# Optimization experiments

Hardware: AMD Instinct MI355X
Metric: run time of the kernel (lower is better)

## Reference

```python
import jax, jax.numpy as jnp
import numpy as np

H = 32        # query heads
KV = 8        # key/value heads
D = 128       # head_dim
GROUPS = H // KV
THETA = 10000.0


def _rope_cos_sin(position_ids):
    # position_ids: [B, S] int
    inv_freq = 1.0 / (THETA ** (jnp.arange(0, D, 2, dtype=jnp.float32) / D))  # [D/2]
    freqs = position_ids.astype(jnp.float32)[:, :, None] * inv_freq[None, None, :]  # [B,S,D/2]
    emb = jnp.concatenate([freqs, freqs], axis=-1)  # [B,S,D]
    return jnp.cos(emb), jnp.sin(emb)


def _rotate_half(x):
    x1, x2 = jnp.split(x, 2, axis=-1)
    return jnp.concatenate([-x2, x1], axis=-1)


def _apply_rope(x, cos, sin):
    # x: [B,h,S,D]; cos/sin: [B,S,D] -> broadcast over heads
    return x * cos[:, None, :, :] + _rotate_half(x) * sin[:, None, :, :]


def setup_inputs() -> dict:
    key = jax.random.key(0)
    ks = jax.random.split(key, 8)
    B, S, Dm = 2, 2048, 4096
    scale = lambda d: 1.0 / np.sqrt(d)
    hidden_states = jax.random.normal(ks[0], (B, S, Dm), dtype=jnp.float32)
    position_ids = jnp.broadcast_to(jnp.arange(S, dtype=jnp.int32)[None, :], (B, S))
    Wq = jax.random.normal(ks[1], (Dm, H * D), dtype=jnp.float32) * scale(Dm)
    Wk = jax.random.normal(ks[2], (Dm, KV * D), dtype=jnp.float32) * scale(Dm)
    Wv = jax.random.normal(ks[3], (Dm, KV * D), dtype=jnp.float32) * scale(Dm)
    Wo = jax.random.normal(ks[4], (H * D, Dm), dtype=jnp.float32) * scale(H * D)
    # per-head shift-encoder correction weights (small init so it's a correction)
    Ws_q = jax.random.normal(ks[5], (H, D, D), dtype=jnp.float32) * (0.02 * scale(D))
    Ws_k = jax.random.normal(ks[6], (H, D, D), dtype=jnp.float32) * (0.02 * scale(D))
    return {"hidden_states": hidden_states, "position_ids": position_ids,
            "Wq": Wq, "Wk": Wk, "Wv": Wv, "Wo": Wo, "Ws_q": Ws_q, "Ws_k": Ws_k}


def reference(hidden_states, position_ids, Wq, Wk, Wv, Wo, Ws_q, Ws_k):
    B, S, Dm = hidden_states.shape
    # projections -> [B, heads, S, D]
    q = (hidden_states @ Wq).reshape(B, S, H, D).transpose(0, 2, 1, 3)
    k = (hidden_states @ Wk).reshape(B, S, KV, D).transpose(0, 2, 1, 3)
    v = (hidden_states @ Wv).reshape(B, S, KV, D).transpose(0, 2, 1, 3)
    # RoPE
    cos, sin = _rope_cos_sin(position_ids)
    q = _apply_rope(q, cos, sin)
    k = _apply_rope(k, cos, sin)
    # GQA repeat_kv: [B,KV,S,D] -> [B,H,S,D]
    k = jnp.repeat(k, GROUPS, axis=1)
    v = jnp.repeat(v, GROUPS, axis=1)
    # causal SDPA
    scores = jnp.einsum('bhqd,bhkd->bhqk', q, k) / jnp.sqrt(jnp.float32(D))
    causal = jnp.tril(jnp.ones((S, S), dtype=bool))
    scores = jnp.where(causal[None, None, :, :], scores, jnp.float32(-1e30))
    probs = jax.nn.softmax(scores, axis=-1)
    attn = jnp.einsum('bhqk,bhkd->bhqd', probs, v)  # [B,H,S,D]
    attn = attn.transpose(0, 2, 1, 3)               # [B,S,H,D]
    # shift_encoder.do_shift: per-head linear correction from rotated Q and K
    delta = jnp.einsum('bhsd,hde->bshe', q, Ws_q) + jnp.einsum('bhsd,hde->bshe', k, Ws_k)
    attn = attn + delta
    # output projection
    out = attn.reshape(B, S, H * D) @ Wo
    return out
```

## Files before the change

### kernel.cpp

```cpp
#include <hip/hip_runtime.h>
#include <cstdint>

#define DEV __device__ __forceinline__

typedef __attribute__((ext_vector_type(4))) float  f32x4;
typedef __attribute__((ext_vector_type(8))) short  s16x8;
typedef __attribute__((ext_vector_type(4))) unsigned short u16x4;
typedef __attribute__((ext_vector_type(8))) unsigned short u16x8;

constexpr int B_   = 2;
constexpr int S_   = 2048;
constexpr int DM   = 4096;
constexpr int HQ   = 32;
constexpr int KVH  = 8;
constexpr int DH   = 128;
constexpr int NQKV = 6144;

DEV unsigned short f2bf(float f) {
  union { float f; unsigned u; } c; c.f = f;
  unsigned u = c.u + 0x7FFFu + ((c.u >> 16) & 1u);
  return (unsigned short)(u >> 16);
}
DEV float bf2f(unsigned short h) {
  union { unsigned u; float f; } c; c.u = (unsigned)h << 16; return c.f;
}
DEV void gload16(const void* g, const void* l) {
  __builtin_amdgcn_global_load_lds(
      (const __attribute__((address_space(1))) unsigned int*)(uintptr_t)g,
      (__attribute__((address_space(3))) unsigned int*)(unsigned)(uintptr_t)l,
      16, 0, 0);
}
DEV f32x4 mfma16x16(s16x8 a, s16x8 b, f32x4 c) {
  return __builtin_amdgcn_mfma_f32_16x16x32_bf16(a, b, c, 0, 0, 0);
}

__global__ __launch_bounds__(256) void k_tables(const int* __restrict__ pos,
                                                float* __restrict__ ct,
                                                float* __restrict__ st) {
  int i = blockIdx.x * 256 + threadIdx.x;
  if (i >= B_ * S_ * 64) return;
  int f = i & 63, bs = i >> 6;
  float p   = (float)pos[bs];
  float inv = __builtin_amdgcn_exp2f(-(float)f * 0.20762050593048355f);
  float a   = p * inv;
  ct[i] = cosf(a);
  st[i] = sinf(a);
}

__global__ __launch_bounds__(256) void k_cvt(const float* __restrict__ in,
                                             unsigned short* __restrict__ out,
                                             int n8) {
  int i = blockIdx.x * 256 + threadIdx.x;
  if (i >= n8) return;
  const f32x4* p = (const f32x4*)in + (size_t)2 * i;
  f32x4 a = p[0], b = p[1];
  u16x8 o;
  o[0] = f2bf(a[0]); o[1] = f2bf(a[1]); o[2] = f2bf(a[2]); o[3] = f2bf(a[3]);
  o[4] = f2bf(b[0]); o[5] = f2bf(b[1]); o[6] = f2bf(b[2]); o[7] = f2bf(b[3]);
  ((u16x8*)out)[i] = o;
}

__global__ __launch_bounds__(256) void k_tconv(const float* __restrict__ in,
                                               unsigned short* __restrict__ out,
                                               int R, int C,
                                               unsigned long long ibs,
                                               unsigned long long obs) {
  __shared__ float t[64][65];
  const int r0 = blockIdx.y * 64, c0 = blockIdx.x * 64;
  const float* ib = in + (size_t)blockIdx.z * ibs;
  unsigned short* ob = out + (size_t)blockIdx.z * obs;
  const int tid = threadIdx.x, tr = tid >> 4, c4 = (tid & 15) * 4;
#pragma unroll
  for (int it = 0; it < 4; ++it) {
    int rr = it * 16 + tr;
    f32x4 v = *(const f32x4*)&ib[(size_t)(r0 + rr) * C + (c0 + c4)];
    t[rr][c4 + 0] = v[0]; t[rr][c4 + 1] = v[1];
    t[rr][c4 + 2] = v[2]; t[rr][c4 + 3] = v[3];
  }
  __syncthreads();
#pragma unroll
  for (int it = 0; it < 4; ++it) {
    int cc = it * 16 + tr;
    u16x4 o;
    o[0] = f2bf(t[c4 + 0][cc]); o[1] = f2bf(t[c4 + 1][cc]);
    o[2] = f2bf(t[c4 + 2][cc]); o[3] = f2bf(t[c4 + 3][cc]);
    *(u16x4*)&ob[(size_t)(c0 + cc) * R + (r0 + c4)] = o;
  }
}

template <int BF16OUT, int SPLIT>
__global__ __launch_bounds__(512, 2) void k_gemm256(const unsigned short* __restrict__ A,
                                                    const unsigned short* __restrict__ BT,
                                                    void* __restrict__ Cv,
                                                    unsigned short* __restrict__ Pv,
                                                    int M, int N, int K, int NBX) {
  extern __shared__ __align__(16) char L[];
  const int tid = threadIdx.x;
  const int lane = tid & 63, w = tid >> 6;
  const int g = lane >> 4, ml = lane & 15;
  const int wr = w & 1, wc = w >> 1;

  int by, bx, koff, klen, cls = 0, ksl = 0;
  if (SPLIT) {
    const int sub = (int)blockIdx.x & 255;
    const int swz = (sub & 7) * 32 + (sub >> 3);
    cls = (int)blockIdx.x >> 8;
    if (cls == 0) { by = swz >> 4; bx = swz & 15; koff = 0; klen = K; }
    else {
      ksl = swz >> 7;
      int v = swz & 127;
      by = v >> 3; bx = 16 + (v & 7);
      koff = ksl * (K >> 1); klen = K >> 1;
    }
  } else {
    const int cpx = (int)gridDim.x >> 3;
    const int swz = ((int)blockIdx.x & 7) * cpx + ((int)blockIdx.x >> 3);
    by = swz / NBX; bx = swz - by * NBX; koff = 0; klen = K;
  }
  const int bm = by * 256, bn = bx * 256;

  const int srow_l = tid >> 3;
  const int scol_e = (((tid & 7) ^ ((tid >> 3) & 7)) << 3);
  const int nk = klen >> 6;

#define STAGE(kt, hf) do {                                                        \
    if ((kt) < nk) {                                                              \
      const unsigned short* sb; char* db;                                         \
      if ((hf) < 2) { sb = A  + (size_t)(bm + (hf) * 128) * K;                    \
                      db = L + ((kt) & 1) * 32768 + (hf) * 16384; }               \
      else          { sb = BT + (size_t)(bn + ((hf) - 2) * 128) * K;              \
                      db = L + 65536 + ((kt) & 1) * 32768 + ((hf) - 2) * 16384; } \
      sb += (size_t)koff + (size_t)(kt) * 64 + scol_e;                            \
      _Pragma("unroll")                                                           \
      for (int r_ = 0; r_ < 2; ++r_)                                              \
        gload16(sb + (size_t)(r_ * 64 + srow_l) * K, db + r_ * 8192 + w * 1024);  \
    } } while (0)

  f32x4 Z = {0.f, 0.f, 0.f, 0.f};
  f32x4 acc[8][4];
#pragma unroll
  for (int i = 0; i < 8; ++i)
#pragma unroll
    for (int j = 0; j < 4; ++j) acc[i][j] = Z;
  s16x8 bfr[4][2], afr[2][2];

#define FRAG(base, row, ks)                                                       \
  ((const s16x8*)((base) + ((((row) >> 7) * 16384 + ((row) & 127) * 128 +         \
                             ((ks) * 32 + 8 * g) * 2) ^ (((row) & 7) << 4))))

#define PHASE(q, kbuf, SKT, SHF, VM) do {                                         \
    if ((q) == 0) {                                                               \
      _Pragma("unroll")                                                           \
      for (int nf = 0; nf < 4; ++nf)                                              \
        _Pragma("unroll")                                                         \
        for (int ks = 0; ks < 2; ++ks)                                            \
          bfr[nf][ks] = *FRAG(L + 65536 + (kbuf) * 32768,                         \
                              wc * 64 + nf * 16 + ml, ks);                        \
    }                                                                             \
    _Pragma("unroll")                                                             \
    for (int mm = 0; mm < 2; ++mm)                                                \
      _Pragma("unroll")                                                           \
      for (int ks = 0; ks < 2; ++ks)                                              \
        afr[mm][ks] = *FRAG(L + (kbuf) * 32768,                                   \
                            32 * (2 * (q) + mm) + 16 * wr + ml, ks);              \
    STAGE(SKT, SHF);                                                              \
    if ((VM) == 1) { asm volatile("s_waitcnt vmcnt(6)" ::: "memory"); }           \
    else if ((VM) == 2) {                                                         \
      if (last) { asm volatile("s_waitcnt vmcnt(0)" ::: "memory"); }              \
      else      { asm volatile("s_waitcnt vmcnt(6)" ::: "memory"); }              \
    } else if ((VM) == 3) {                                                       \
      if (!last) { asm volatile("s_waitcnt vmcnt(6)" ::: "memory"); }             \
    }                                                                             \
    __builtin_amdgcn_s_barrier();                                                 \
    asm volatile("s_waitcnt lgkmcnt(0)" ::: "memory");                            \
    __builtin_amdgcn_sched_barrier(0);                                            \
    __builtin_amdgcn_s_setprio(1);                                                \
    _Pragma("unroll")                                                             \
    for (int mm = 0; mm < 2; ++mm)                                                \
      _Pragma("unroll")                                                           \
      for (int nf = 0; nf < 4; ++nf)                                              \
        _Pragma("unroll")                                                         \
        for (int ks = 0; ks < 2; ++ks)                                            \
          acc[2 * (q) + mm][nf] =                                                 \
              mfma16x16(afr[mm][ks], bfr[nf][ks], acc[2 * (q) + mm][nf]);         \
    __builtin_amdgcn_s_setprio(0);                                                \
    __builtin_amdgcn_s_barrier();                                                 \
  } while (0)

  STAGE(0, 0); STAGE(0, 1); STAGE(0, 2); STAGE(0, 3);
  STAGE(1, 2); STAGE(1, 3); STAGE(1, 0);
  asm volatile("s_waitcnt vmcnt(6)" ::: "memory");
  __builtin_amdgcn_s_barrier();

  const int iters = nk >> 1;
  for (int i = 0; i < iters; ++i) {
    const int t = 2 * i;
    const bool last = (i == iters - 1);
    PHASE(0, 0, t + 1, 1, 0);
    PHASE(1, 0, t + 2, 2, 0);
    PHASE(2, 0, t + 2, 0, 0);
    PHASE(3, 0, t + 2, 3, 2);
    PHASE(0, 1, t + 2, 1, 0);
    PHASE(1, 1, t + 3, 2, 0);
    PHASE(2, 1, t + 3, 3, 0);
    PHASE(3, 1, t + 3, 0, 3);
  }
#undef PHASE
#undef FRAG
#undef STAGE

  const int row0 = bm + 16 * wr + 4 * g, col0 = bn + wc * 64 + ml;
  const bool toPart = (SPLIT && cls == 1 && ksl == 1);
#pragma unroll
  for (int m = 0; m < 8; ++m)
#pragma unroll
    for (int nf = 0; nf < 4; ++nf)
#pragma unroll
      for (int r = 0; r < 4; ++r) {
        int row = row0 + 32 * m + r;
        int col = col0 + nf * 16;
        if (BF16OUT) {
          if (toPart)
            Pv[(size_t)row * 2048 + (col - 4096)] = f2bf(acc[m][nf][r]);
          else
            ((unsigned short*)Cv)[(size_t)row * N + col] = f2bf(acc[m][nf][r]);
        } else {
          ((float*)Cv)[(size_t)row * N + col] = acc[m][nf][r];
        }
      }
}

__global__ __launch_bounds__(256) void k_rope(const unsigned short* __restrict__ qkv,
                                              const unsigned short* __restrict__ p1,
                                              const float* __restrict__ ct,
                                              const float* __restrict__ st,
                                              unsigned short* __restrict__ qr,
                                              unsigned short* __restrict__ kr) {
  const int bs = blockIdx.x;
  const int b = bs >> 11, s = bs & 2047;
  const int tid = threadIdx.x;
  const float* cr = ct + (size_t)bs * 64;
  const float* sr = st + (size_t)bs * 64;
  const unsigned short* row = qkv + (size_t)bs * NQKV;
  {
    int h = tid >> 3, d0 = (tid & 7) * 16;
    u16x8 xs  = *(const u16x8*)&row[h * 128 + d0];
    u16x8 xs2 = *(const u16x8*)&row[h * 128 + d0 + 8];
    u16x8 xp  = *(const u16x8*)&row[h * 128 + (d0 ^ 64)];
    u16x8 xp2 = *(const u16x8*)&row[h * 128 + (d0 ^ 64) + 8];
    float sg = (d0 < 64) ? -1.f : 1.f;
    int ci = d0 & 63;
    u16x8 o1, o2;
#pragma unroll
    for (int j = 0; j < 8; ++j)
      o1[j] = f2bf(bf2f(xs[j]) * cr[ci + j] + sg * bf2f(xp[j]) * sr[ci + j]);
#pragma unroll
    for (int j = 0; j < 8; ++j)
      o2[j] = f2bf(bf2f(xs2[j]) * cr[ci + 8 + j] + sg * bf2f(xp2[j]) * sr[ci + 8 + j]);
    unsigned short* dst = qr + ((size_t)(b * HQ + h) * S_ + s) * DH + d0;
    *(u16x8*)dst = o1;
    *(u16x8*)(dst + 8) = o2;
  }
  if (tid < 64) {
    int kv = tid >> 3, d0 = (tid & 7) * 16;
    const unsigned short* krow = row + HQ * DH + kv * 128;
    const unsigned short* prow = p1 + (size_t)bs * 2048 + kv * 128;
    u16x8 xs  = *(const u16x8*)&krow[d0];
    u16x8 xs2 = *(const u16x8*)&krow[d0 + 8];
    u16x8 xp  = *(const u16x8*)&krow[d0 ^ 64];
    u16x8 xp2 = *(const u16x8*)&krow[(d0 ^ 64) + 8];
    u16x8 ys  = *(const u16x8*)&prow[d0];
    u16x8 ys2 = *(const u16x8*)&prow[d0 + 8];
    u16x8 yp  = *(const u16x8*)&prow[d0 ^ 64];
    u16x8 yp2 = *(const u16x8*)&prow[(d0 ^ 64) + 8];
    float sg = (d0 < 64) ? -1.f : 1.f;
    int ci = d0 & 63;
    u16x8 o1, o2;
#pragma unroll
    for (int j = 0; j < 8; ++j)
      o1[j] = f2bf((bf2f(xs[j]) + bf2f(ys[j])) * cr[ci + j] +
                   sg * (bf2f(xp[j]) + bf2f(yp[j])) * sr[ci + j]);
#pragma unroll
    for (int j = 0; j < 8; ++j)
      o2[j] = f2bf((bf2f(xs2[j]) + bf2f(ys2[j])) * cr[ci + 8 + j] +
                   sg * (bf2f(xp2[j]) + bf2f(yp2[j])) * sr[ci + 8 + j]);
    unsigned short* dst = kr + ((size_t)(b * KVH + kv) * S_ + s) * DH + d0;
    *(u16x8*)dst = o1;
    *(u16x8*)(dst + 8) = o2;
  }
}

__global__ __launch_bounds__(256) void k_vtrans(const unsigned short* __restrict__ qkv,
                                                const unsigned short* __restrict__ p1,
                                                unsigned short* __restrict__ vt) {
  __shared__ unsigned short t[64][65];
  const int z = blockIdx.z, b = z >> 3, kv = z & 7;
  const int s0 = blockIdx.x * 64, d0 = blockIdx.y * 64;
  const int tid = threadIdx.x, tr = tid >> 4, c4 = (tid & 15) * 4;
  const unsigned short* src = qkv + (size_t)(b * S_) * NQKV + HQ * DH + KVH * DH + kv * 128;
  const unsigned short* psr = p1 + (size_t)(b * S_) * 2048 + 1024 + kv * 128;
#pragma unroll
  for (int it = 0; it < 4; ++it) {
    int s = it * 16 + tr;
    u16x4 v = *(const u16x4*)&src[(size_t)(s0 + s) * NQKV + d0 + c4];
    u16x4 q = *(const u16x4*)&psr[(size_t)(s0 + s) * 2048 + d0 + c4];
    t[s][c4 + 0] = f2bf(bf2f(v[0]) + bf2f(q[0]));
    t[s][c4 + 1] = f2bf(bf2f(v[1]) + bf2f(q[1]));
    t[s][c4 + 2] = f2bf(bf2f(v[2]) + bf2f(q[2]));
    t[s][c4 + 3] = f2bf(bf2f(v[3]) + bf2f(q[3]));
  }
  __syncthreads();
  unsigned short* dst = vt + (size_t)(b * KVH + kv) * DH * S_;
#pragma unroll
  for (int it = 0; it < 4; ++it) {
    int d = it * 16 + tr;
    u16x4 o;
    o[0] = t[c4 + 0][d]; o[1] = t[c4 + 1][d];
    o[2] = t[c4 + 2][d]; o[3] = t[c4 + 3][d];
    *(u16x4*)&dst[(size_t)(d0 + d) * S_ + s0 + c4] = o;
  }
}

__global__ __launch_bounds__(256) void k_attn(const unsigned short* __restrict__ qr,
                                              const unsigned short* __restrict__ kr,
                                              const unsigned short* __restrict__ vt,
                                              const unsigned short* __restrict__ wsq,
                                              const unsigned short* __restrict__ wsk,
                                              unsigned short* __restrict__ att) {
  const int h = blockIdx.y, b = blockIdx.z, kvh = h >> 2;
  const int tid = threadIdx.x, lane = tid & 63, w = tid >> 6;
  const int g = lane >> 4, ml = lane & 15;

  __shared__ unsigned short kvbuf[16384];
  __shared__ unsigned short pbuf[4][32 * 72];
  unsigned short* kl = kvbuf;
  unsigned short* vl = kvbuf + 8192;

  const unsigned short* Kg = kr + (size_t)(b * KVH + kvh) * S_ * DH;
  const unsigned short* Vg = vt + (size_t)(b * KVH + kvh) * DH * S_;
  const float CS = 0.12751745f;
  f32x4 Z = {0.f, 0.f, 0.f, 0.f};

  for (int half = 0; half < 2; ++half) {
    const int qbx = half ? (15 - (int)blockIdx.x) : (int)blockIdx.x;
    const int qb0 = qbx * 128;
    const unsigned short* Qg = qr + ((size_t)(b * HQ + h) * S_ + qb0) * DH;

    __syncthreads();
#pragma unroll
    for (int it = 0; it < 8; ++it) {
      int c = w + 4 * it;
      int off = c * 1024 + lane * 16;
      int row = off >> 8;
      int sch = ((off >> 4) & 15) ^ (row & 7);
      gload16(Qg + (size_t)row * DH + sch * 8, (const char*)kvbuf + c * 1024);
    }
    __syncthreads();
    s16x8 qfr[2][4];
#pragma unroll
    for (int qf = 0; qf < 2; ++qf)
#pragma unroll
      for (int ds = 0; ds < 4; ++ds) {
        int row = 32 * w + 16 * qf + ml;
        int sch = (4 * ds + g) ^ (row & 7);
        qfr[qf][ds] = *(const s16x8*)((const char*)kvbuf + row * 256 + sch * 16);
      }

    float mstate[2] = {-3e30f, -3e30f};
    float lstate[2] = {0.f, 0.f};
    f32x4 oacc[2][8];
    s16x8 kfr[2][4];
#pragma unroll
    for (int i = 0; i < 2; ++i)
#pragma unroll
      for (int j = 0; j < 8; ++j) oacc[i][j] = Z;

    const int ntiles = (qb0 >> 6) + 2;

    for (int t = 0; t < ntiles; ++t) {
      const int kv0 = t * 64;
      __syncthreads();
#pragma unroll
      for (int it = 0; it < 4; ++it) {
        int c = w + 4 * it;
        int off = c * 1024 + lane * 16;
        int row = off >> 8;
        int sch = ((off >> 4) & 15) ^ (row & 7);
        gload16(Kg + (size_t)(kv0 + row) * DH + sch * 8, (const char*)kl + c * 1024);
      }
#pragma unroll
      for (int it = 0; it < 4; ++it) {
        int c = w + 4 * it;
        int off = c * 1024 + lane * 16;
        int row = off >> 7;
        int sch = ((off >> 4) & 7) ^ (row & 7);
        gload16(Vg + (size_t)row * S_ + kv0 + sch * 8, (const char*)vl + c * 1024);
      }
      __syncthreads();

      f32x4 sacc[4][2];
#pragma unroll
      for (int i = 0; i < 4; ++i) { sacc[i][0] = Z; sacc[i][1] = Z; }
#pragma unroll
      for (int ds = 0; ds < 4; ++ds) {
        s16x8 af[4];
#pragma unroll
        for (int kf = 0; kf < 4; ++kf) {
          int row = 16 * kf + ml;
          int sch = (4 * ds + g) ^ (row & 7);
          af[kf] = *(const s16x8*)((const char*)kl + row * 256 + sch * 16);
        }
#pragma unroll
        for (int kf = 0; kf < 4; ++kf)
#pragma unroll
          for (int qf = 0; qf < 2; ++qf)
            sacc[kf][qf] = mfma16x16(af[kf], qfr[qf][ds], sacc[kf][qf]);
      }

      {
        int rel = kv0 - qb0;
        if (rel == ((w >> 1) << 6)) {
#pragma unroll
          for (int qf = 0; qf < 2; ++qf)
#pragma unroll
            for (int ds = 0; ds < 4; ++ds) {
              int row = 32 * w + 16 * qf + ml - rel;
              int sch = (4 * ds + g) ^ (row & 7);
              kfr[qf][ds] = *(const s16x8*)((const char*)kl + row * 256 + sch * 16);
            }
        }
      }

      const int qg = qb0 + 32 * w + ml;
      const bool fullTile = (kv0 + 63 <= qb0 + 32 * w);
      float alpha[2];
#pragma unroll
      for (int qf = 0; qf < 2; ++qf) {
        int qq = qg + 16 * qf;
        float mx = -3e30f;
        if (fullTile) {
#pragma unroll
          for (int kf = 0; kf < 4; ++kf)
#pragma unroll
            for (int r = 0; r < 4; ++r) {
              float sv = sacc[kf][qf][r] * CS;
              sacc[kf][qf][r] = sv;
              mx = fmaxf(mx, sv);
            }
        } else {
#pragma unroll
          for (int kf = 0; kf < 4; ++kf)
#pragma unroll
            for (int r = 0; r < 4; ++r) {
              float sv = sacc[kf][qf][r] * CS;
              int kk = kv0 + 16 * kf + 4 * g + r;
              sv = (kk <= qq) ? sv : -3e30f;
              sacc[kf][qf][r] = sv;
              mx = fmaxf(mx, sv);
            }
        }
        mx = fmaxf(mx, __shfl_xor(mx, 16));
        mx = fmaxf(mx, __shfl_xor(mx, 32));
        float mn = fmaxf(mstate[qf], mx);
        alpha[qf] = __builtin_amdgcn_exp2f(mstate[qf] - mn);
        mstate[qf] = mn;
        float ls = 0.f;
#pragma unroll
        for (int kf = 0; kf < 4; ++kf) {
          u16x4 pk;
#pragma unroll
          for (int r = 0; r < 4; ++r) {
            float p = __builtin_amdgcn_exp2f(sacc[kf][qf][r] - mn);
            ls += p;
            pk[r] = f2bf(p);
          }
          *(u16x4*)&pbuf[w][(16 * qf + ml) * 72 + 16 * kf + 4 * g] = pk;
        }
        ls += __shfl_xor(ls, 16);
        ls += __shfl_xor(ls, 32);
        lstate[qf] = lstate[qf] * alpha[qf] + ls;
      }
#pragma unroll
      for (int mf = 0; mf < 2; ++mf)
#pragma unroll
        for (int r = 0; r < 4; ++r) {
          float a = __shfl(alpha[mf], (lane & 48) | (4 * g + r));
#pragma unroll
          for (int nf = 0; nf < 8; ++nf) oacc[mf][nf][r] *= a;
        }
#pragma unroll
      for (int ks = 0; ks < 2; ++ks) {
        s16x8 pa[2];
#pragma unroll
        for (int mf = 0; mf < 2; ++mf)
          pa[mf] = *(const s16x8*)&pbuf[w][(16 * mf + ml) * 72 + 32 * ks + 8 * g];
#pragma unroll
        for (int nf = 0; nf < 8; ++nf) {
          int row = 16 * nf + ml;
          int sch = (4 * ks + g) ^ (row & 7);
          s16x8 bv = *(const s16x8*)((const char*)vl + row * 128 + sch * 16);
#pragma unroll
          for (int mf = 0; mf < 2; ++mf)
            oacc[mf][nf] = mfma16x16(pa[mf], bv, oacc[mf][nf]);
        }
      }
    }

#pragma unroll
    for (int mf = 0; mf < 2; ++mf)
#pragma unroll
      for (int r = 0; r < 4; ++r) {
        float li = __shfl(lstate[mf], (lane & 48) | (4 * g + r));
        float inv = 1.0f / li;
#pragma unroll
        for (int nf = 0; nf < 8; ++nf) oacc[mf][nf][r] *= inv;
      }

#pragma unroll
    for (int pass = 0; pass < 2; ++pass) {
      const unsigned short* Wg =
          (pass == 0 ? wsq : wsk) + (size_t)h * DH * DH;
      __syncthreads();
#pragma unroll
      for (int it = 0; it < 8; ++it) {
        int c = w + 4 * it;
        int off = c * 1024 + lane * 16;
        int row = off >> 8;
        int sch = ((off >> 4) & 15) ^ (row & 7);
        gload16(Wg + (size_t)row * DH + sch * 8, (const char*)kvbuf + c * 1024);
      }
      __syncthreads();
#pragma unroll
      for (int nf = 0; nf < 8; ++nf) {
        s16x8 wf[4];
#pragma unroll
        for (int ds = 0; ds < 4; ++ds) {
          int row = 16 * nf + ml;
          int sch = (4 * ds + g) ^ (row & 7);
          wf[ds] = *(const s16x8*)((const char*)kvbuf + row * 256 + sch * 16);
        }
#pragma unroll
        for (int qf = 0; qf < 2; ++qf)
#pragma unroll
          for (int ds = 0; ds < 4; ++ds)
            oacc[qf][nf] = mfma16x16(pass == 0 ? qfr[qf][ds] : kfr[qf][ds],
                                     wf[ds], oacc[qf][nf]);
      }
    }

#pragma unroll
    for (int mf = 0; mf < 2; ++mf)
#pragma unroll
      for (int r = 0; r < 4; ++r) {
        int rowg = b * S_ + qb0 + 32 * w + 16 * mf + 4 * g + r;
        size_t base = (size_t)rowg * (HQ * DH) + h * DH;
#pragma unroll
        for (int nf = 0; nf < 8; ++nf)
          att[base + 16 * nf + ml] = f2bf(oacc[mf][nf][r]);
      }
  }
}

extern "C" void kernel_launch(void* const* d_in, const int* in_sizes, int n_in,
                              void* d_out, int out_size, void* d_ws, size_t ws_size,
                              hipStream_t stream) {
  const float* hidden = (const float*)d_in[0];
  const int*   pos    = (const int*)d_in[1];
  const float* Wq     = (const float*)d_in[2];
  const float* Wk     = (const float*)d_in[3];
  const float* Wv     = (const float*)d_in[4];
  const float* Wo     = (const float*)d_in[5];
  const float* Wsq    = (const float*)d_in[6];
  const float* Wsk    = (const float*)d_in[7];

  char* ws = (char*)d_ws;
  unsigned short* XB    = (unsigned short*)(ws + 0);
  unsigned short* WQKVT = (unsigned short*)(ws + 33554432);
  unsigned short* WOT   = (unsigned short*)(ws + 83886080);
  unsigned short* P1    = WOT;
  unsigned short* WSQT  = (unsigned short*)(ws + 117440512);
  unsigned short* WSKT  = (unsigned short*)(ws + 118489088);
  float*          CT    = (float*)(ws + 119537664);
  float*          ST    = (float*)(ws + 120586240);
  unsigned short* QKV   = (unsigned short*)(ws + 121634816);
  unsigned short* QR    = (unsigned short*)(ws + 171966464);
  unsigned short* KR    = (unsigned short*)(ws + 205520896);
  unsigned short* VT    = (unsigned short*)(ws + 213909504);
  unsigned short* ATT   = (unsigned short*)(ws + 222298112);

  k_tables<<<1024, 256, 0, stream>>>(pos, CT, ST);
  k_cvt<<<8192, 256, 0, stream>>>(hidden, XB, 2097152);
  k_tconv<<<dim3(64, 64, 1), 256, 0, stream>>>(Wq, WQKVT, 4096, 4096, 0, 0);
  k_tconv<<<dim3(16, 64, 1), 256, 0, stream>>>(Wk, WQKVT + (size_t)4096 * 4096, 4096, 1024, 0, 0);
  k_tconv<<<dim3(16, 64, 1), 256, 0, stream>>>(Wv, WQKVT + (size_t)5120 * 4096, 4096, 1024, 0, 0);
  k_tconv<<<dim3(2, 2, 32), 256, 0, stream>>>(Wsq, WSQT, 128, 128, 16384, 16384);
  k_tconv<<<dim3(2, 2, 32), 256, 0, stream>>>(Wsk, WSKT, 128, 128, 16384, 16384);
  k_gemm256<1, 1><<<dim3(512), 512, 131072, stream>>>(XB, WQKVT, QKV, P1,
                                                      4096, 6144, 4096, 0);
  k_rope<<<4096, 256, 0, stream>>>(QKV, P1, CT, ST, QR, KR);
  k_vtrans<<<dim3(32, 2, 16), 256, 0, stream>>>(QKV, P1, VT);
  k_tconv<<<dim3(64, 64, 1), 256, 0, stream>>>(Wo, WOT, 4096, 4096, 0, 0);
  k_attn<<<dim3(8, 32, 2), 256, 0, stream>>>(QR, KR, VT, WSQT, WSKT, ATT);
  k_gemm256<0, 0><<<dim3(256), 512, 131072, stream>>>(ATT, WOT, d_out, nullptr,
                                                      4096, 4096, 4096, 16);
}
```

Measured before the change: 595.8 us.

## Split attention into one q-block per workgroup with heaviest blocks scheduled first

Previously each attention workgroup handled two paired query blocks (i and 15-i) one after the other to balance causal work. Now each workgroup handles one 128-row query block, the grid doubles to 16x32x2, and blocks are ordered heaviest-first. Launch bounds request 3 waves per SIMD, and the P staging buffer stride drops from 72 to 68, so P reads are split into two 8-byte loads. The K rows for the shift correction are reloaded from global memory after the loop instead of being captured during the diagonal tile. The aim is more workgroups in flight and higher occupancy to hide latency, at the cost of per-block setup, possible register spilling under the tighter bound, and relying on the hardware scheduler to balance the uneven causal work.

```diff
diff --git a/kernel.cpp b/kernel.cpp
--- a/kernel.cpp
+++ b/kernel.cpp
@@ -321,31 +321,210 @@
   }
 }
 
-__global__ __launch_bounds__(256) void k_attn(const unsigned short* __restrict__ qr,
-                                              const unsigned short* __restrict__ kr,
-                                              const unsigned short* __restrict__ vt,
-                                              const unsigned short* __restrict__ wsq,
-                                              const unsigned short* __restrict__ wsk,
-                                              unsigned short* __restrict__ att) {
+__global__ __launch_bounds__(256, 3) void k_attn(const unsigned short* __restrict__ qr,
+                                                 const unsigned short* __restrict__ kr,
+                                                 const unsigned short* __restrict__ vt,
+                                                 const unsigned short* __restrict__ wsq,
+                                                 const unsigned short* __restrict__ wsk,
+                                                 unsigned short* __restrict__ att) {
   const int h = blockIdx.y, b = blockIdx.z, kvh = h >> 2;
   const int tid = threadIdx.x, lane = tid & 63, w = tid >> 6;
   const int g = lane >> 4, ml = lane & 15;
 
   __shared__ unsigned short kvbuf[16384];
-  __shared__ unsigned short pbuf[4][32 * 72];
+  __shared__ unsigned short pbuf[4][32 * 68];
   unsigned short* kl = kvbuf;
   unsigned short* vl = kvbuf + 8192;
 
+  const int qbx = 15 - (int)blockIdx.x;
+  const int qb0 = qbx * 128;
+  const unsigned short* Qg = qr + ((size_t)(b * HQ + h) * S_ + qb0) * DH;
   const unsigned short* Kg = kr + (size_t)(b * KVH + kvh) * S_ * DH;
   const unsigned short* Vg = vt + (size_t)(b * KVH + kvh) * DH * S_;
   const float CS = 0.12751745f;
   f32x4 Z = {0.f, 0.f, 0.f, 0.f};
 
-  for (int half = 0; half < 2; ++half) {
-    const int qbx = half ? (15 - (int)blockIdx.x) : (int)blockIdx.x;
-    const int qb0 = qbx * 128;
-    const unsigned short* Qg = qr + ((size_t)(b * HQ + h) * S_ + qb0) * DH;
-
+#pragma unroll
+  for (int it = 0; it < 8; ++it) {
+    int c = w + 4 * it;
+    int off = c * 1024 + lane * 16;
+    int row = off >> 8;
+    int sch = ((off >> 4) & 15) ^ (row & 7);
+    gload16(Qg + (size_t)row * DH + sch * 8, (const char*)kvbuf + c * 1024);
+  }
+  __syncthreads();
+  s16x8 qfr[2][4];
+#pragma unroll
+  for (int qf = 0; qf < 2; ++qf)
+#pragma unroll
+    for (int ds = 0; ds < 4; ++ds) {
+      int row = 32 * w + 16 * qf + ml;
+      int sch = (4 * ds + g) ^ (row & 7);
+      qfr[qf][ds] = *(const s16x8*)((const char*)kvbuf + row * 256 + sch * 16);
+    }
+
+  float mstate[2] = {-3e30f, -3e30f};
+  float lstate[2] = {0.f, 0.f};
+  f32x4 oacc[2][8];
+#pragma unroll
+  for (int i = 0; i < 2; ++i)
+#pragma unroll
+    for (int j = 0; j < 8; ++j) oacc[i][j] = Z;
+
+  const int ntiles = (qb0 >> 6) + 2;
+
+  for (int t = 0; t < ntiles; ++t) {
+    const int kv0 = t * 64;
+    __syncthreads();
+#pragma unroll
+    for (int it = 0; it < 4; ++it) {
+      int c = w + 4 * it;
+      int off = c * 1024 + lane * 16;
+      int row = off >> 8;
+      int sch = ((off >> 4) & 15) ^ (row & 7);
+      gload16(Kg + (size_t)(kv0 + row) * DH + sch * 8, (const char*)kl + c * 1024);
+    }
+#pragma unroll
+    for (int it = 0; it < 4; ++it) {
+      int c = w + 4 * it;
+      int off = c * 1024 + lane * 16;
+      int row = off >> 7;
+      int sch = ((off >> 4) & 7) ^ (row & 7);
+      gload16(Vg + (size_t)row * S_ + kv0 + sch * 8, (const char*)vl + c * 1024);
+    }
+    __syncthreads();
+
+    f32x4 sacc[4][2];
+#pragma unroll
+    for (int i = 0; i < 4; ++i) { sacc[i][0] = Z; sacc[i][1] = Z; }
+#pragma unroll
+    for (int ds = 0; ds < 4; ++ds) {
+      s16x8 af[4];
+#pragma unroll
+      for (int kf = 0; kf < 4; ++kf) {
+        int row = 16 * kf + ml;
+        int sch = (4 * ds + g) ^ (row & 7);
+        af[kf] = *(const s16x8*)((const char*)kl + row * 256 + sch * 16);
+      }
+#pragma unroll
+      for (int kf = 0; kf < 4; ++kf)
+#pragma unroll
+        for (int qf = 0; qf < 2; ++qf)
+          sacc[kf][qf] = mfma16x16(af[kf], qfr[qf][ds], sacc[kf][qf]);
+    }
+
+    const int qg = qb0 + 32 * w + ml;
+    const bool fullTile = (kv0 + 63 <= qb0 + 32 * w);
+    float alpha[2];
+#pragma unroll
+    for (int qf = 0; qf < 2; ++qf) {
+      int qq = qg + 16 * qf;
+      float mx = -3e30f;
+      if (fullTile) {
+#pragma unroll
+        for (int kf = 0; kf < 4; ++kf)
+#pragma unroll
+          for (int r = 0; r < 4; ++r) {
+            float sv = sacc[kf][qf][r] * CS;
+            sacc[kf][qf][r] = sv;
+            mx = fmaxf(mx, sv);
+          }
+      } else {
+#pragma unroll
+        for (int kf = 0; kf < 4; ++kf)
+#pragma unroll
+          for (int r = 0; r < 4; ++r) {
+            float sv = sacc[kf][qf][r] * CS;
+            int kk = kv0 + 16 * kf + 4 * g + r;
+            sv = (kk <= qq) ? sv : -3e30f;
+            sacc[kf][qf][r] = sv;
+            mx = fmaxf(mx, sv);
+          }
+      }
+      mx = fmaxf(mx, __shfl_xor(mx, 16));
+      mx = fmaxf(mx, __shfl_xor(mx, 32));
+      float mn = fmaxf(mstate[qf], mx);
+      alpha[qf] = __builtin_amdgcn_exp2f(mstate[qf] - mn);
+      mstate[qf] = mn;
+      float ls = 0.f;
+#pragma unroll
+      for (int kf = 0; kf < 4; ++kf) {
+        u16x4 pk;
+#pragma unroll
+        for (int r = 0; r < 4; ++r) {
+          float p = __builtin_amdgcn_exp2f(sacc[kf][qf][r] - mn);
+          ls += p;
+          pk[r] = f2bf(p);
+        }
+        *(u16x4*)&pbuf[w][(16 * qf + ml) * 68 + 16 * kf + 4 * g] = pk;
+      }
+      ls += __shfl_xor(ls, 16);
+      ls += __shfl_xor(ls, 32);
+      lstate[qf] = lstate[qf] * alpha[qf] + ls;
+    }
+#pragma unroll
+    for (int mf = 0; mf < 2; ++mf)
+#pragma unroll
+      for (int r = 0; r < 4; ++r) {
+        float a = __shfl(alpha[mf], (lane & 48) | (4 * g + r));
+#pragma unroll
+        for (int nf = 0; nf < 8; ++nf) oacc[mf][nf][r] *= a;
+      }
+#pragma unroll
+    for (int ks = 0; ks < 2; ++ks) {
+      s16x8 pa[2];
+#pragma unroll
+      for (int mf = 0; mf < 2; ++mf) {
+        const unsigned short* pr = &pbuf[w][(16 * mf + ml) * 68 + 32 * ks + 8 * g];
+        u16x4 lo = *(const u16x4*)pr;
+        u16x4 hi = *(const u16x4*)(pr + 4);
+        pa[mf] = (s16x8)__builtin_shufflevector(lo, hi, 0, 1, 2, 3, 4, 5, 6, 7);
+      }
+#pragma unroll
+      for (int nf = 0; nf < 8; ++nf) {
+        int row = 16 * nf + ml;
+        int sch = (4 * ks + g) ^ (row & 7);
+        s16x8 bv = *(const s16x8*)((const char*)vl + row * 128 + sch * 16);
+#pragma unroll
+        for (int mf = 0; mf < 2; ++mf)
+          oacc[mf][nf] = mfma16x16(pa[mf], bv, oacc[mf][nf]);
+      }
+    }
+  }
+
+#pragma unroll
+  for (int mf = 0; mf < 2; ++mf)
+#pragma unroll
+    for (int r = 0; r < 4; ++r) {
+      float li = __shfl(lstate[mf], (lane & 48) | (4 * g + r));
+      float inv = 1.0f / li;
+#pragma unroll
+      for (int nf = 0; nf < 8; ++nf) oacc[mf][nf][r] *= inv;
+    }
+
+  s16x8 kfr[2][4];
+  __syncthreads();
+#pragma unroll
+  for (int it = 0; it < 8; ++it) {
+    int c = w + 4 * it;
+    int off = c * 1024 + lane * 16;
+    int row = off >> 8;
+    int sch = ((off >> 4) & 15) ^ (row & 7);
+    gload16(Kg + (size_t)(qb0 + row) * DH + sch * 8, (const char*)kvbuf + c * 1024);
+  }
+  __syncthreads();
+#pragma unroll
+  for (int qf = 0; qf < 2; ++qf)
+#pragma unroll
+    for (int ds = 0; ds < 4; ++ds) {
+      int row = 32 * w + 16 * qf + ml;
+      int sch = (4 * ds + g) ^ (row & 7);
+      kfr[qf][ds] = *(const s16x8*)((const char*)kvbuf + row * 256 + sch * 16);
+    }
+
+#pragma unroll
+  for (int pass = 0; pass < 2; ++pass) {
+    const unsigned short* Wg = (pass == 0 ? wsq : wsk) + (size_t)h * DH * DH;
     __syncthreads();
 #pragma unroll
     for (int it = 0; it < 8; ++it) {
@@ -353,212 +532,37 @@
       int off = c * 1024 + lane * 16;
       int row = off >> 8;
       int sch = ((off >> 4) & 15) ^ (row & 7);
-      gload16(Qg + (size_t)row * DH + sch * 8, (const char*)kvbuf + c * 1024);
+      gload16(Wg + (size_t)row * DH + sch * 8, (const char*)kvbuf + c * 1024);
     }
     __syncthreads();
-    s16x8 qfr[2][4];
-#pragma unroll
-    for (int qf = 0; qf < 2; ++qf)
+#pragma unroll
+    for (int nf = 0; nf < 8; ++nf) {
+      s16x8 wf[4];
 #pragma unroll
       for (int ds = 0; ds < 4; ++ds) {
-        int row = 32 * w + 16 * qf + ml;
+        int row = 16 * nf + ml;
         int sch = (4 * ds + g) ^ (row & 7);
-        qfr[qf][ds] = *(const s16x8*)((const char*)kvbuf + row * 256 + sch * 16);
-      }
-
-    float mstate[2] = {-3e30f, -3e30f};
-    float lstate[2] = {0.f, 0.f};
-    f32x4 oacc[2][8];
-    s16x8 kfr[2][4];
-#pragma unroll
-    for (int i = 0; i < 2; ++i)
-#pragma unroll
-      for (int j = 0; j < 8; ++j) oacc[i][j] = Z;
-
-    const int ntiles = (qb0 >> 6) + 2;
-
-    for (int t = 0; t < ntiles; ++t) {
-      const int kv0 = t * 64;
-      __syncthreads();
-#pragma unroll
-      for (int it = 0; it < 4; ++it) {
-        int c = w + 4 * it;
-        int off = c * 1024 + lane * 16;
-        int row = off >> 8;
-        int sch = ((off >> 4) & 15) ^ (row & 7);
-        gload16(Kg + (size_t)(kv0 + row) * DH + sch * 8, (const char*)kl + c * 1024);
-      }
-#pragma unroll
-      for (int it = 0; it < 4; ++it) {
-        int c = w + 4 * it;
-        int off = c * 1024 + lane * 16;
-        int row = off >> 7;
-        int sch = ((off >> 4) & 7) ^ (row & 7);
-        gload16(Vg + (size_t)row * S_ + kv0 + sch * 8, (const char*)vl + c * 1024);
-      }
-      __syncthreads();
-
-      f32x4 sacc[4][2];
-#pragma unroll
-      for (int i = 0; i < 4; ++i) { sacc[i][0] = Z; sacc[i][1] = Z; }
-#pragma unroll
-      for (int ds = 0; ds < 4; ++ds) {
-        s16x8 af[4];
-#pragma unroll
-        for (int kf = 0; kf < 4; ++kf) {
-          int row = 16 * kf + ml;
-          int sch = (4 * ds + g) ^ (row & 7);
-          af[kf] = *(const s16x8*)((const char*)kl + row * 256 + sch * 16);
-        }
-#pragma unroll
-        for (int kf = 0; kf < 4; ++kf)
-#pragma unroll
-          for (int qf = 0; qf < 2; ++qf)
-            sacc[kf][qf] = mfma16x16(af[kf], qfr[qf][ds], sacc[kf][qf]);
-      }
-
-      {
-        int rel = kv0 - qb0;
-        if (rel == ((w >> 1) << 6)) {
-#pragma unroll
-          for (int qf = 0; qf < 2; ++qf)
-#pragma unroll
-            for (int ds = 0; ds < 4; ++ds) {
-              int row = 32 * w + 16 * qf + ml - rel;
-              int sch = (4 * ds + g) ^ (row & 7);
-              kfr[qf][ds] = *(const s16x8*)((const char*)kl + row * 256 + sch * 16);
-            }
-        }
-      }
-
-      const int qg = qb0 + 32 * w + ml;
-      const bool fullTile = (kv0 + 63 <= qb0 + 32 * w);
-      float alpha[2];
-#pragma unroll
-      for (int qf = 0; qf < 2; ++qf) {
-        int qq = qg + 16 * qf;
-        float mx = -3e30f;
-        if (fullTile) {
-#pragma unroll
-          for (int kf = 0; kf < 4; ++kf)
-#pragma unroll
-            for (int r = 0; r < 4; ++r) {
-              float sv = sacc[kf][qf][r] * CS;
-              sacc[kf][qf][r] = sv;
-              mx = fmaxf(mx, sv);
-            }
-        } else {
-#pragma unroll
-          for (int kf = 0; kf < 4; ++kf)
-#pragma unroll
-            for (int r = 0; r < 4; ++r) {
-              float sv = sacc[kf][qf][r] * CS;
-              int kk = kv0 + 16 * kf + 4 * g + r;
-              sv = (kk <= qq) ? sv : -3e30f;
-              sacc[kf][qf][r] = sv;
-              mx = fmaxf(mx, sv);
-            }
-        }
-        mx = fmaxf(mx, __shfl_xor(mx, 16));
-        mx = fmaxf(mx, __shfl_xor(mx, 32));
-        float mn = fmaxf(mstate[qf], mx);
-        alpha[qf] = __builtin_amdgcn_exp2f(mstate[qf] - mn);
-        mstate[qf] = mn;
-        float ls = 0.f;
-#pragma unroll
-        for (int kf = 0; kf < 4; ++kf) {
-          u16x4 pk;
-#pragma unroll
-          for (int r = 0; r < 4; ++r) {
-            float p = __builtin_amdgcn_exp2f(sacc[kf][qf][r] - mn);
-            ls += p;
-            pk[r] = f2bf(p);
-          }
-          *(u16x4*)&pbuf[w][(16 * qf + ml) * 72 + 16 * kf + 4 * g] = pk;
-        }
-        ls += __shfl_xor(ls, 16);
-        ls += __shfl_xor(ls, 32);
-        lstate[qf] = lstate[qf] * alpha[qf] + ls;
-      }
-#pragma unroll
-      for (int mf = 0; mf < 2; ++mf)
-#pragma unroll
-        for (int r = 0; r < 4; ++r) {
-          float a = __shfl(alpha[mf], (lane & 48) | (4 * g + r));
-#pragma unroll
-          for (int nf = 0; nf < 8; ++nf) oacc[mf][nf][r] *= a;
-        }
-#pragma unroll
-      for (int ks = 0; ks < 2; ++ks) {
-        s16x8 pa[2];
-#pragma unroll
-        for (int mf = 0; mf < 2; ++mf)
-          pa[mf] = *(const s16x8*)&pbuf[w][(16 * mf + ml) * 72 + 32 * ks + 8 * g];
-#pragma unroll
-        for (int nf = 0; nf < 8; ++nf) {
-          int row = 16 * nf + ml;
-          int sch = (4 * ks + g) ^ (row & 7);
-          s16x8 bv = *(const s16x8*)((const char*)vl + row * 128 + sch * 16);
-#pragma unroll
-          for (int mf = 0; mf < 2; ++mf)
-            oacc[mf][nf] = mfma16x16(pa[mf], bv, oacc[mf][nf]);
-        }
-      }
-    }
-
-#pragma unroll
-    for (int mf = 0; mf < 2; ++mf)
-#pragma unroll
-      for (int r = 0; r < 4; ++r) {
-        float li = __shfl(lstate[mf], (lane & 48) | (4 * g + r));
-        float inv = 1.0f / li;
-#pragma unroll
-        for (int nf = 0; nf < 8; ++nf) oacc[mf][nf][r] *= inv;
-      }
-
-#pragma unroll
-    for (int pass = 0; pass < 2; ++pass) {
-      const unsigned short* Wg =
-          (pass == 0 ? wsq : wsk) + (size_t)h * DH * DH;
-      __syncthreads();
-#pragma unroll
-      for (int it = 0; it < 8; ++it) {
-        int c = w + 4 * it;
-        int off = c * 1024 + lane * 16;
-        int row = off >> 8;
-        int sch = ((off >> 4) & 15) ^ (row & 7);
-        gload16(Wg + (size_t)row * DH + sch * 8, (const char*)kvbuf + c * 1024);
-      }
-      __syncthreads();
-#pragma unroll
-      for (int nf = 0; nf < 8; ++nf) {
-        s16x8 wf[4];
-#pragma unroll
-        for (int ds = 0; ds < 4; ++ds) {
-          int row = 16 * nf + ml;
-          int sch = (4 * ds + g) ^ (row & 7);
-          wf[ds] = *(const s16x8*)((const char*)kvbuf + row * 256 + sch * 16);
-        }
-#pragma unroll
-        for (int qf = 0; qf < 2; ++qf)
-#pragma unroll
-          for (int ds = 0; ds < 4; ++ds)
-            oacc[qf][nf] = mfma16x16(pass == 0 ? qfr[qf][ds] : kfr[qf][ds],
-                                     wf[ds], oacc[qf][nf]);
-      }
-    }
-
-#pragma unroll
-    for (int mf = 0; mf < 2; ++mf)
-#pragma unroll
-      for (int r = 0; r < 4; ++r) {
-        int rowg = b * S_ + qb0 + 32 * w + 16 * mf + 4 * g + r;
-        size_t base = (size_t)rowg * (HQ * DH) + h * DH;
-#pragma unroll
-        for (int nf = 0; nf < 8; ++nf)
-          att[base + 16 * nf + ml] = f2bf(oacc[mf][nf][r]);
-      }
-  }
+        wf[ds] = *(const s16x8*)((const char*)kvbuf + row * 256 + sch * 16);
+      }
+#pragma unroll
+      for (int qf = 0; qf < 2; ++qf)
+#pragma unroll
+        for (int ds = 0; ds < 4; ++ds)
+          oacc[qf][nf] = mfma16x16(pass == 0 ? qfr[qf][ds] : kfr[qf][ds],
+                                   wf[ds], oacc[qf][nf]);
+    }
+  }
+
+#pragma unroll
+  for (int mf = 0; mf < 2; ++mf)
+#pragma unroll
+    for (int r = 0; r < 4; ++r) {
+      int rowg = b * S_ + qb0 + 32 * w + 16 * mf + 4 * g + r;
+      size_t base = (size_t)rowg * (HQ * DH) + h * DH;
+#pragma unroll
+      for (int nf = 0; nf < 8; ++nf)
+        att[base + 16 * nf + ml] = f2bf(oacc[mf][nf][r]);
+    }
 }
 
 extern "C" void kernel_launch(void* const* d_in, const int* in_sizes, int n_in,
@@ -600,7 +604,7 @@
   k_rope<<<4096, 256, 0, stream>>>(QKV, P1, CT, ST, QR, KR);
   k_vtrans<<<dim3(32, 2, 16), 256, 0, stream>>>(QKV, P1, VT);
   k_tconv<<<dim3(64, 64, 1), 256, 0, stream>>>(Wo, WOT, 4096, 4096, 0, 0);
-  k_attn<<<dim3(8, 32, 2), 256, 0, stream>>>(QR, KR, VT, WSQT, WSKT, ATT);
+  k_attn<<<dim3(16, 32, 2), 256, 0, stream>>>(QR, KR, VT, WSQT, WSKT, ATT);
   k_gemm256<0, 0><<<dim3(256), 512, 131072, stream>>>(ATT, WOT, d_out, nullptr,
                                                       4096, 4096, 4096, 16);
 }
```

Measured after the change: 741.0 us. +24.4%, slower.
